# Kernel optimization log

Measured on AMD Instinct MI355X. Metric: run time of the kernel, lower is better.

The kernel has to match this reference:

```python
import jax, jax.numpy as jnp
import numpy as np

N_SRC = 50000   # source nodes in the block
N_DST = 50000   # destination nodes
E = 800000      # edges (avg in-degree 16, every dst has >=1 edge)
D = 256         # hidden_dim
V = 50000       # vocab_size
C = 104         # n_classes (POJ-104)


def setup_inputs() -> dict:
    key = jax.random.key(0)
    k1, k2, k3, k4, k5, k6 = jax.random.split(key, 6)
    token_id = jax.random.randint(k1, (N_SRC,), 0, V, dtype=jnp.int32)
    src_idx = jax.random.randint(k2, (E,), 0, N_SRC, dtype=jnp.int32)
    # every dst node gets at least one in-edge (DGL raises on 0-in-degree),
    # remaining edges land on random dst nodes; sorted so edges are grouped by dst
    extra = jax.random.randint(k3, (E - N_DST,), 0, N_DST, dtype=jnp.int32)
    dst_idx = jnp.sort(jnp.concatenate([jnp.arange(N_DST, dtype=jnp.int32), extra]))
    emb = jax.random.normal(k4, (V, D), dtype=jnp.float32)  # nn.Embedding default N(0,1)
    W = jax.random.normal(k5, (D, D), dtype=jnp.float32) / jnp.sqrt(D)
    b = jnp.zeros((D,), dtype=jnp.float32)
    Wc = jax.random.normal(k6, (C, D), dtype=jnp.float32) / jnp.sqrt(D)
    bc = jnp.zeros((C,), dtype=jnp.float32)
    return {"emb": emb, "W": W, "b": b, "Wc": Wc, "bc": bc,
            "token_id": token_id, "src_idx": src_idx, "dst_idx": dst_idx}


def reference(emb, W, b, Wc, bc, token_id, src_idx, dst_idx):
    # embedding gather for source nodes (first_layer branch)
    feat_src = emb[token_id]                  # [N_SRC, D]
    # message: copy_u -> mailbox messages per edge
    msgs = feat_src[src_idx]                  # [E, D]
    # per-dst segment stats (dst_idx is sorted / grouped by dst)
    deg = jax.ops.segment_sum(jnp.ones((E,), dtype=jnp.int32), dst_idx,
                              num_segments=N_DST)            # [N_DST]
    sum_all = jax.ops.segment_sum(msgs, dst_idx, num_segments=N_DST)  # [N_DST, D]
    # DGL mailbox reducer: last message in the segment is the 'current input',
    # the rest are children summed through CodeRNNCell: x = cur + relu(W @ sum_children + b)
    last_idx = jnp.cumsum(deg) - 1            # index of last edge per dst segment
    last_msg = msgs[last_idx]                 # [N_DST, D]
    child_sum = sum_all - last_msg            # sum of msgs excluding the last one
    rnn_out = last_msg + jax.nn.relu(child_sum @ W.T + b)
    # length == 1 segments bypass the RNN cell entirely: ft = the single message
    ft = jnp.where((deg == 1)[:, None], last_msg, rnn_out)   # [N_DST, D]
    # final classifier
    return ft @ Wc.T + bc                     # [N_DST, C]
```

## Files before the change

kernel.cpp:

```cpp
#include <hip/hip_runtime.h>
#include <hip/hip_bf16.h>

#define DD 256
#define CC 104

typedef __bf16 bf16x8 __attribute__((ext_vector_type(8)));
typedef float  f32x4  __attribute__((ext_vector_type(4)));

__device__ inline float bu2f(unsigned short u) {
    return __uint_as_float(((unsigned)u) << 16);
}
__device__ inline unsigned short f2bu(float f) {
    __hip_bfloat16 h = __float2bfloat16(f);
    return *reinterpret_cast<unsigned short*>(&h);
}

__global__ void prep_all(
    const int* __restrict__ token_id,
    const int* __restrict__ src_idx,
    const int* __restrict__ dst_idx,
    int* __restrict__ seg_start,
    int* __restrict__ seg_end,
    int* __restrict__ edge_tok,
    int E, int PB,
    const float* __restrict__ W,
    const float* __restrict__ Wc,
    __hip_bfloat16* __restrict__ Wfrag,
    __hip_bfloat16* __restrict__ Wcfrag)
{
    const int b = blockIdx.x;
    const int t = threadIdx.x;
    if (b < PB) {
        int e = b * 256 + t;
        if (e >= E) return;
        int d = dst_idx[e];
        edge_tok[e] = token_id[src_idx[e]];
        if (e == 0 || dst_idx[e - 1] != d) seg_start[d] = e;
        if (e == E - 1 || dst_idx[e + 1] != d) seg_end[d] = e + 1;
        return;
    }
    if (b < PB + 32) {
        int idx  = (b - PB) * 256 + t;
        int lane = idx & 63, g = idx >> 6;
        int nt = g & 15, k0 = g >> 4;
        int r = nt * 16 + (lane & 15);
        int c = k0 * 32 + (lane >> 4) * 8;
        const float* src = W + (size_t)r * DD + c;
        float4 v0 = *(const float4*)(src);
        float4 v1 = *(const float4*)(src + 4);
        uint4 pk;
        pk.x = (unsigned)f2bu(v0.x) | ((unsigned)f2bu(v0.y) << 16);
        pk.y = (unsigned)f2bu(v0.z) | ((unsigned)f2bu(v0.w) << 16);
        pk.z = (unsigned)f2bu(v1.x) | ((unsigned)f2bu(v1.y) << 16);
        pk.w = (unsigned)f2bu(v1.z) | ((unsigned)f2bu(v1.w) << 16);
        *(uint4*)(Wfrag + (size_t)idx * 8) = pk;
        return;
    }
    {
        int idx  = (b - PB - 32) * 256 + t;
        int lane = idx & 63, g = idx >> 6;
        int nt = g & 7, k0 = g >> 3;
        int r = nt * 16 + (lane & 15);
        int c = k0 * 32 + (lane >> 4) * 8;
        float4 v0 = make_float4(0.f,0.f,0.f,0.f);
        float4 v1 = make_float4(0.f,0.f,0.f,0.f);
        if (r < CC) {
            const float* src = Wc + (size_t)r * DD + c;
            v0 = *(const float4*)(src);
            v1 = *(const float4*)(src + 4);
        }
        uint4 pk;
        pk.x = (unsigned)f2bu(v0.x) | ((unsigned)f2bu(v0.y) << 16);
        pk.y = (unsigned)f2bu(v0.z) | ((unsigned)f2bu(v0.w) << 16);
        pk.z = (unsigned)f2bu(v1.x) | ((unsigned)f2bu(v1.y) << 16);
        pk.w = (unsigned)f2bu(v1.z) | ((unsigned)f2bu(v1.w) << 16);
        *(uint4*)(Wcfrag + (size_t)idx * 8) = pk;
    }
}

__global__ __launch_bounds__(256, 3) void we_gemm(
    const float* __restrict__ emb,
    const __hip_bfloat16* __restrict__ Wfrag,
    __hip_bfloat16* __restrict__ Webuf,
    __hip_bfloat16* __restrict__ embb,
    int V)
{
    __shared__ __hip_bfloat16 lds[32 * 512];
    const int t    = threadIdx.x;
    const int lane = t & 63;
    const int w    = t >> 6;
    const int quad = lane >> 4;
    const int l16  = lane & 15;
    const int mrow = blockIdx.x * 64 + w * 16 + l16;
    const int row  = min(mrow, V - 1);

    bf16x8 bfrag[8];
#pragma unroll
    for (int k0 = 0; k0 < 8; ++k0) {
        const float* src = emb + (size_t)row * DD + k0 * 32 + quad * 8;
        float4 v0 = *(const float4*)(src);
        float4 v1 = *(const float4*)(src + 4);
        uint4 pk;
        pk.x = (unsigned)f2bu(v0.x) | ((unsigned)f2bu(v0.y) << 16);
        pk.y = (unsigned)f2bu(v0.z) | ((unsigned)f2bu(v0.w) << 16);
        pk.z = (unsigned)f2bu(v1.x) | ((unsigned)f2bu(v1.y) << 16);
        pk.w = (unsigned)f2bu(v1.z) | ((unsigned)f2bu(v1.w) << 16);
        bfrag[k0] = *(bf16x8*)&pk;
        if (mrow < V)
            *(uint4*)(embb + (size_t)row * DD + k0 * 32 + quad * 8) = pk;
    }

    f32x4 acc[16];
#pragma unroll
    for (int nt = 0; nt < 16; ++nt) acc[nt] = (f32x4){0.f,0.f,0.f,0.f};

    for (int p = 0; p < 4; ++p) {
        if (p) __syncthreads();
#pragma unroll
        for (int it = 0; it < 8; ++it) {
            int idx = it * 256 + t;
            *(uint4*)(lds + (size_t)idx * 8) =
                *(const uint4*)(Wfrag + (size_t)p * 16384 + (size_t)idx * 8);
        }
        __syncthreads();
#pragma unroll
        for (int kl = 0; kl < 2; ++kl) {
            int k0 = p * 2 + kl;
#pragma unroll
            for (int nt = 0; nt < 16; ++nt) {
                bf16x8 wf = *(const bf16x8*)(lds + (kl * 16 + nt) * 512 + lane * 8);
                acc[nt] = __builtin_amdgcn_mfma_f32_16x16x32_bf16(wf, bfrag[k0], acc[nt], 0, 0, 0);
            }
        }
    }

    if (mrow < V) {
#pragma unroll
        for (int nt = 0; nt < 16; ++nt) {
            ushort4 o;
            o.x = f2bu(acc[nt][0]);
            o.y = f2bu(acc[nt][1]);
            o.z = f2bu(acc[nt][2]);
            o.w = f2bu(acc[nt][3]);
            *(ushort4*)(Webuf + (size_t)mrow * DD + nt * 16 + quad * 4) = o;
        }
    }
}

__global__ __launch_bounds__(256, 8) void seg_rnn_kernel(
                               const __hip_bfloat16* __restrict__ Webuf,
                               const __hip_bfloat16* __restrict__ embb,
                               const int* __restrict__ edge_tok,
                               const int* __restrict__ seg_start,
                               const int* __restrict__ seg_end,
                               const float* __restrict__ bvec,
                               __hip_bfloat16* __restrict__ ftb,
                               int n_dst)
{
    int w = (blockIdx.x * blockDim.x + threadIdx.x) >> 6;
    int lane = threadIdx.x & 63;
    if (w >= n_dst) return;
    int h   = lane >> 5;
    int l32 = lane & 31;
    int s  = seg_start[w];
    int e  = seg_end[w];
    int n  = e - 1 - s;
    int lt = edge_tok[e - 1];
    uint4 lm = *(const uint4*)(embb + (size_t)lt * DD + l32 * 8);
    bool gate = n > 0;
    int nfast = n < 64 ? n : 64;
    float acc[8] = {0.f,0.f,0.f,0.f,0.f,0.f,0.f,0.f};

#pragma unroll
    for (int bb = 0; bb < 4; ++bb) {
        int base = bb * 16;
        if (nfast > base) {
            uint4 uu[8];
#pragma unroll
            for (int k = 0; k < 8; ++k) {
                int r  = base + 2 * k + h;
                int rc = r < n - 1 ? r : n - 1;
                int tk = edge_tok[s + rc];
                uu[k] = *(const uint4*)(Webuf + (size_t)tk * DD + l32 * 8);
            }
#pragma unroll
            for (int k = 0; k < 8; ++k) {
                int r = base + 2 * k + h;
                if (r < nfast) {
                    const unsigned* ud = (const unsigned*)&uu[k];
#pragma unroll
                    for (int d = 0; d < 4; ++d) {
                        acc[2*d]   += __uint_as_float(ud[d] << 16);
                        acc[2*d+1] += __uint_as_float(ud[d] & 0xffff0000u);
                    }
                }
            }
        }
    }
    for (int i = s + 64 + h; i < e - 1; i += 2) {
        int t0 = edge_tok[i];
        uint4 u = *(const uint4*)(Webuf + (size_t)t0 * DD + l32 * 8);
        const unsigned* ud = (const unsigned*)&u;
#pragma unroll
        for (int d = 0; d < 4; ++d) {
            acc[2*d]   += __uint_as_float(ud[d] << 16);
            acc[2*d+1] += __uint_as_float(ud[d] & 0xffff0000u);
        }
    }

#pragma unroll
    for (int j = 0; j < 8; ++j) acc[j] += __shfl_xor(acc[j], 32, 64);

    if (h == 0) {
        float4 b0 = *(const float4*)(bvec + l32 * 8);
        float4 b1 = *(const float4*)(bvec + l32 * 8 + 4);
        float bl[8] = {b0.x, b0.y, b0.z, b0.w, b1.x, b1.y, b1.z, b1.w};
        const unsigned* lmd = (const unsigned*)&lm;
        uint4 o;
        unsigned* od = (unsigned*)&o;
#pragma unroll
        for (int d = 0; d < 4; ++d) {
            float lo = __uint_as_float(lmd[d] << 16);
            float hi = __uint_as_float(lmd[d] & 0xffff0000u);
            float v0 = lo + (gate ? fmaxf(acc[2*d]   + bl[2*d],   0.f) : 0.f);
            float v1 = hi + (gate ? fmaxf(acc[2*d+1] + bl[2*d+1], 0.f) : 0.f);
            od[d] = (unsigned)f2bu(v0) | ((unsigned)f2bu(v1) << 16);
        }
        *(uint4*)(ftb + (size_t)w * DD + l32 * 8) = o;
    }
}

__global__ __launch_bounds__(256, 4) void cls_mfma(
    const __hip_bfloat16* __restrict__ ftb,
    const __hip_bfloat16* __restrict__ Wcfrag,
    const float* __restrict__ bc,
    float* __restrict__ out,
    int M)
{
    __shared__ __hip_bfloat16 lds[32 * 512];
    const int t    = threadIdx.x;
    const int lane = t & 63;
    const int w    = t >> 6;
    const int quad = lane >> 4;
    const int l16  = lane & 15;
    const int mw   = blockIdx.x * 64 + w * 16;

    int mrow = min(mw + l16, M - 1);
    bf16x8 ffrag[8];
    const __hip_bfloat16* arow = ftb + (size_t)mrow * DD + quad * 8;
#pragma unroll
    for (int k0 = 0; k0 < 8; ++k0)
        ffrag[k0] = *(const bf16x8*)(arow + k0 * 32);

    f32x4 acc[8];
#pragma unroll
    for (int nt = 0; nt < 8; ++nt) acc[nt] = (f32x4){0.f,0.f,0.f,0.f};

    for (int p = 0; p < 2; ++p) {
        if (p) __syncthreads();
#pragma unroll
        for (int it = 0; it < 8; ++it) {
            int idx = it * 256 + t;
            *(uint4*)(lds + (size_t)idx * 8) =
                *(const uint4*)(Wcfrag + (size_t)p * 16384 + (size_t)idx * 8);
        }
        __syncthreads();
#pragma unroll
        for (int kl = 0; kl < 4; ++kl) {
            int k0 = p * 4 + kl;
#pragma unroll
            for (int nt = 0; nt < 8; ++nt) {
                bf16x8 wf = *(const bf16x8*)(lds + (kl * 8 + nt) * 512 + lane * 8);
                acc[nt] = __builtin_amdgcn_mfma_f32_16x16x32_bf16(wf, ffrag[k0], acc[nt], 0, 0, 0);
            }
        }
    }

    int m = mw + l16;
    if (m < M) {
#pragma unroll
        for (int nt = 0; nt < 8; ++nt) {
            int c0 = nt * 16 + quad * 4;
            if (c0 <= 100) {
                float4 bia = *(const float4*)(bc + c0);
                float4 o;
                o.x = acc[nt][0] + bia.x;
                o.y = acc[nt][1] + bia.y;
                o.z = acc[nt][2] + bia.z;
                o.w = acc[nt][3] + bia.w;
                *(float4*)(out + (size_t)m * CC + c0) = o;
            }
        }
    }
}

extern "C" void kernel_launch(void* const* d_in, const int* in_sizes, int n_in,
                              void* d_out, int out_size, void* d_ws, size_t ws_size,
                              hipStream_t stream)
{
    const float* emb      = (const float*)d_in[0];
    const float* W        = (const float*)d_in[1];
    const float* bvec     = (const float*)d_in[2];
    const float* Wc       = (const float*)d_in[3];
    const float* bc       = (const float*)d_in[4];
    const int*   token_id = (const int*)d_in[5];
    const int*   src_idx  = (const int*)d_in[6];
    const int*   dst_idx  = (const int*)d_in[7];
    float*       out      = (float*)d_out;

    const int E     = in_sizes[6];
    const int Vemb  = in_sizes[0] / DD;
    const int n_dst = out_size / CC;
    (void)n_in; (void)ws_size;

    char* ws = (char*)d_ws;
    size_t off = 0;
    auto alloc = [&](size_t bytes) {
        void* p = ws + off;
        off = (off + bytes + 255) & ~(size_t)255;
        return p;
    };
    int* seg_start = (int*)alloc((size_t)n_dst * sizeof(int));
    int* seg_end   = (int*)alloc((size_t)n_dst * sizeof(int));
    int* edge_tok  = (int*)alloc((size_t)E * sizeof(int));
    __hip_bfloat16* embb   = (__hip_bfloat16*)alloc((size_t)Vemb * DD * 2);
    __hip_bfloat16* Webuf  = (__hip_bfloat16*)alloc((size_t)Vemb * DD * 2);
    __hip_bfloat16* ftb    = (__hip_bfloat16*)alloc((size_t)n_dst * DD * 2);
    __hip_bfloat16* Wfrag  = (__hip_bfloat16*)alloc((size_t)128 * 512 * 2);
    __hip_bfloat16* Wcfrag = (__hip_bfloat16*)alloc((size_t)64 * 512 * 2);

    const int PB = (E + 255) / 256;
    const int we_blocks  = (Vemb + 63) / 64;
    const int cls_blocks = (n_dst + 63) / 64;

    prep_all<<<PB + 48, 256, 0, stream>>>(
        token_id, src_idx, dst_idx, seg_start, seg_end, edge_tok, E, PB,
        W, Wc, Wfrag, Wcfrag);
    we_gemm<<<we_blocks, 256, 0, stream>>>(
        emb, Wfrag, Webuf, embb, Vemb);
    seg_rnn_kernel<<<(n_dst + 3) / 4, 256, 0, stream>>>(
        Webuf, embb, edge_tok, seg_start, seg_end, bvec, ftb, n_dst);
    cls_mfma<<<cls_blocks, 256, 0, stream>>>(
        ftb, Wcfrag, bc, out, n_dst);
}
```

Measured before the change: 204.7 us.

## Slice feature tables into 32-column panels and gather per slice for L2 locality

Stores the transformed embedding table, bf16 embedding copy and the ft buffer in a column-sliced layout (eight panels of 32 columns each). The segment kernel now assigns each block one slice and has four lanes per destination node, so each panel's gather working set is smaller and may fit better in cache. The last token per segment is precomputed in prep, which saves a dependent load. The cost is that each edge token is reloaded eight times, one per slice, and there are more blocks with divergent loop lengths across the 16 nodes sharing a wave.

```diff
diff --git a/kernel.cpp b/kernel.cpp
--- a/kernel.cpp
+++ b/kernel.cpp
@@ -3,6 +3,7 @@
 
 #define DD 256
 #define CC 104
+#define NSL 8
 
 typedef __bf16 bf16x8 __attribute__((ext_vector_type(8)));
 typedef float  f32x4  __attribute__((ext_vector_type(4)));
@@ -22,6 +23,7 @@
     int* __restrict__ seg_start,
     int* __restrict__ seg_end,
     int* __restrict__ edge_tok,
+    int* __restrict__ last_tok,
     int E, int PB,
     const float* __restrict__ W,
     const float* __restrict__ Wc,
@@ -34,9 +36,10 @@
         int e = b * 256 + t;
         if (e >= E) return;
         int d = dst_idx[e];
-        edge_tok[e] = token_id[src_idx[e]];
+        int tok = token_id[src_idx[e]];
+        edge_tok[e] = tok;
         if (e == 0 || dst_idx[e - 1] != d) seg_start[d] = e;
-        if (e == E - 1 || dst_idx[e + 1] != d) seg_end[d] = e + 1;
+        if (e == E - 1 || dst_idx[e + 1] != d) { seg_end[d] = e + 1; last_tok[d] = tok; }
         return;
     }
     if (b < PB + 32) {
@@ -107,7 +110,7 @@
         pk.w = (unsigned)f2bu(v1.z) | ((unsigned)f2bu(v1.w) << 16);
         bfrag[k0] = *(bf16x8*)&pk;
         if (mrow < V)
-            *(uint4*)(embb + (size_t)row * DD + k0 * 32 + quad * 8) = pk;
+            *(uint4*)(embb + (size_t)k0 * V * 32 + (size_t)row * 32 + quad * 8) = pk;
     }
 
     f32x4 acc[16];
@@ -137,97 +140,93 @@
     if (mrow < V) {
 #pragma unroll
         for (int nt = 0; nt < 16; ++nt) {
+            int c0 = nt * 16 + quad * 4;
             ushort4 o;
             o.x = f2bu(acc[nt][0]);
             o.y = f2bu(acc[nt][1]);
             o.z = f2bu(acc[nt][2]);
             o.w = f2bu(acc[nt][3]);
-            *(ushort4*)(Webuf + (size_t)mrow * DD + nt * 16 + quad * 4) = o;
+            *(ushort4*)(Webuf + (size_t)(c0 >> 5) * V * 32 +
+                        (size_t)mrow * 32 + (c0 & 31)) = o;
         }
     }
 }
 
 __global__ __launch_bounds__(256, 8) void seg_rnn_kernel(
-                               const __hip_bfloat16* __restrict__ Webuf,
-                               const __hip_bfloat16* __restrict__ embb,
-                               const int* __restrict__ edge_tok,
-                               const int* __restrict__ seg_start,
-                               const int* __restrict__ seg_end,
-                               const float* __restrict__ bvec,
-                               __hip_bfloat16* __restrict__ ftb,
-                               int n_dst)
-{
-    int w = (blockIdx.x * blockDim.x + threadIdx.x) >> 6;
-    int lane = threadIdx.x & 63;
-    if (w >= n_dst) return;
-    int h   = lane >> 5;
-    int l32 = lane & 31;
-    int s  = seg_start[w];
-    int e  = seg_end[w];
-    int n  = e - 1 - s;
-    int lt = edge_tok[e - 1];
-    uint4 lm = *(const uint4*)(embb + (size_t)lt * DD + l32 * 8);
+    const __hip_bfloat16* __restrict__ Webuf,
+    const __hip_bfloat16* __restrict__ embb,
+    const int* __restrict__ edge_tok,
+    const int* __restrict__ seg_start,
+    const int* __restrict__ seg_end,
+    const int* __restrict__ last_tok,
+    const float* __restrict__ bvec,
+    __hip_bfloat16* __restrict__ ftb,
+    int n_dst, int V)
+{
+    const int bid  = blockIdx.x;
+    const int sl   = bid & 7;
+    const int g    = bid >> 3;
+    const int t    = threadIdx.x;
+    const int wv   = t >> 6;
+    const int lane = t & 63;
+    const int grp  = lane >> 2;
+    const int c    = lane & 3;
+
+    int d = g * 64 + wv * 16 + grp;
+    bool dok = d < n_dst;
+    int dc = dok ? d : n_dst - 1;
+    int s  = seg_start[dc];
+    int e  = seg_end[dc];
+    int lt = last_tok[dc];
+    int n  = dok ? (e - 1 - s) : 0;
+
+    const __hip_bfloat16* wsl = Webuf + (size_t)sl * V * 32;
+    const __hip_bfloat16* esl = embb  + (size_t)sl * V * 32;
+    uint4 lm = *(const uint4*)(esl + (size_t)lt * 32 + c * 8);
+
+    float acc[8] = {0.f,0.f,0.f,0.f,0.f,0.f,0.f,0.f};
+
+    for (int j = 0; ; j += 2) {
+        bool a0 = j < n, a1 = j + 1 < n;
+        if (!__any(a0)) break;
+        uint4 u0 = make_uint4(0u,0u,0u,0u);
+        uint4 u1 = make_uint4(0u,0u,0u,0u);
+        if (a0) {
+            int t0 = edge_tok[s + j];
+            u0 = *(const uint4*)(wsl + (size_t)t0 * 32 + c * 8);
+        }
+        if (a1) {
+            int t1 = edge_tok[s + j + 1];
+            u1 = *(const uint4*)(wsl + (size_t)t1 * 32 + c * 8);
+        }
+        const unsigned* p0 = (const unsigned*)&u0;
+        const unsigned* p1 = (const unsigned*)&u1;
+#pragma unroll
+        for (int k = 0; k < 4; ++k) {
+            acc[2*k]   += __uint_as_float(p0[k] << 16)
+                        + __uint_as_float(p1[k] << 16);
+            acc[2*k+1] += __uint_as_float(p0[k] & 0xffff0000u)
+                        + __uint_as_float(p1[k] & 0xffff0000u);
+        }
+    }
+
     bool gate = n > 0;
-    int nfast = n < 64 ? n : 64;
-    float acc[8] = {0.f,0.f,0.f,0.f,0.f,0.f,0.f,0.f};
-
-#pragma unroll
-    for (int bb = 0; bb < 4; ++bb) {
-        int base = bb * 16;
-        if (nfast > base) {
-            uint4 uu[8];
-#pragma unroll
-            for (int k = 0; k < 8; ++k) {
-                int r  = base + 2 * k + h;
-                int rc = r < n - 1 ? r : n - 1;
-                int tk = edge_tok[s + rc];
-                uu[k] = *(const uint4*)(Webuf + (size_t)tk * DD + l32 * 8);
-            }
-#pragma unroll
-            for (int k = 0; k < 8; ++k) {
-                int r = base + 2 * k + h;
-                if (r < nfast) {
-                    const unsigned* ud = (const unsigned*)&uu[k];
-#pragma unroll
-                    for (int d = 0; d < 4; ++d) {
-                        acc[2*d]   += __uint_as_float(ud[d] << 16);
-                        acc[2*d+1] += __uint_as_float(ud[d] & 0xffff0000u);
-                    }
-                }
-            }
-        }
-    }
-    for (int i = s + 64 + h; i < e - 1; i += 2) {
-        int t0 = edge_tok[i];
-        uint4 u = *(const uint4*)(Webuf + (size_t)t0 * DD + l32 * 8);
-        const unsigned* ud = (const unsigned*)&u;
-#pragma unroll
-        for (int d = 0; d < 4; ++d) {
-            acc[2*d]   += __uint_as_float(ud[d] << 16);
-            acc[2*d+1] += __uint_as_float(ud[d] & 0xffff0000u);
-        }
-    }
-
-#pragma unroll
-    for (int j = 0; j < 8; ++j) acc[j] += __shfl_xor(acc[j], 32, 64);
-
-    if (h == 0) {
-        float4 b0 = *(const float4*)(bvec + l32 * 8);
-        float4 b1 = *(const float4*)(bvec + l32 * 8 + 4);
-        float bl[8] = {b0.x, b0.y, b0.z, b0.w, b1.x, b1.y, b1.z, b1.w};
-        const unsigned* lmd = (const unsigned*)&lm;
-        uint4 o;
-        unsigned* od = (unsigned*)&o;
-#pragma unroll
-        for (int d = 0; d < 4; ++d) {
-            float lo = __uint_as_float(lmd[d] << 16);
-            float hi = __uint_as_float(lmd[d] & 0xffff0000u);
-            float v0 = lo + (gate ? fmaxf(acc[2*d]   + bl[2*d],   0.f) : 0.f);
-            float v1 = hi + (gate ? fmaxf(acc[2*d+1] + bl[2*d+1], 0.f) : 0.f);
-            od[d] = (unsigned)f2bu(v0) | ((unsigned)f2bu(v1) << 16);
-        }
-        *(uint4*)(ftb + (size_t)w * DD + l32 * 8) = o;
-    }
+    float4 b0 = *(const float4*)(bvec + sl * 32 + c * 8);
+    float4 b1 = *(const float4*)(bvec + sl * 32 + c * 8 + 4);
+    float bl[8] = {b0.x, b0.y, b0.z, b0.w, b1.x, b1.y, b1.z, b1.w};
+    const unsigned* lmd = (const unsigned*)&lm;
+    uint4 o;
+    unsigned* od = (unsigned*)&o;
+#pragma unroll
+    for (int k = 0; k < 4; ++k) {
+        float lo = __uint_as_float(lmd[k] << 16);
+        float hi = __uint_as_float(lmd[k] & 0xffff0000u);
+        float v0 = lo + (gate ? fmaxf(acc[2*k]   + bl[2*k],   0.f) : 0.f);
+        float v1 = hi + (gate ? fmaxf(acc[2*k+1] + bl[2*k+1], 0.f) : 0.f);
+        od[k] = (unsigned)f2bu(v0) | ((unsigned)f2bu(v1) << 16);
+    }
+    if (dok)
+        *(uint4*)(ftb + (size_t)sl * n_dst * 32 + (size_t)d * 32 + c * 8) = o;
 }
 
 __global__ __launch_bounds__(256, 4) void cls_mfma(
@@ -247,10 +246,10 @@
 
     int mrow = min(mw + l16, M - 1);
     bf16x8 ffrag[8];
-    const __hip_bfloat16* arow = ftb + (size_t)mrow * DD + quad * 8;
 #pragma unroll
     for (int k0 = 0; k0 < 8; ++k0)
-        ffrag[k0] = *(const bf16x8*)(arow + k0 * 32);
+        ffrag[k0] = *(const bf16x8*)(ftb + (size_t)k0 * M * 32 +
+                                     (size_t)mrow * 32 + quad * 8);
 
     f32x4 acc[8];
 #pragma unroll
@@ -322,6 +321,7 @@
     };
     int* seg_start = (int*)alloc((size_t)n_dst * sizeof(int));
     int* seg_end   = (int*)alloc((size_t)n_dst * sizeof(int));
+    int* last_tok  = (int*)alloc((size_t)n_dst * sizeof(int));
     int* edge_tok  = (int*)alloc((size_t)E * sizeof(int));
     __hip_bfloat16* embb   = (__hip_bfloat16*)alloc((size_t)Vemb * DD * 2);
     __hip_bfloat16* Webuf  = (__hip_bfloat16*)alloc((size_t)Vemb * DD * 2);
@@ -331,15 +331,17 @@
 
     const int PB = (E + 255) / 256;
     const int we_blocks  = (Vemb + 63) / 64;
+    const int seg_blocks = NSL * ((n_dst + 63) / 64);
     const int cls_blocks = (n_dst + 63) / 64;
 
     prep_all<<<PB + 48, 256, 0, stream>>>(
-        token_id, src_idx, dst_idx, seg_start, seg_end, edge_tok, E, PB,
+        token_id, src_idx, dst_idx, seg_start, seg_end, edge_tok, last_tok, E, PB,
         W, Wc, Wfrag, Wcfrag);
     we_gemm<<<we_blocks, 256, 0, stream>>>(
         emb, Wfrag, Webuf, embb, Vemb);
-    seg_rnn_kernel<<<(n_dst + 3) / 4, 256, 0, stream>>>(
-        Webuf, embb, edge_tok, seg_start, seg_end, bvec, ftb, n_dst);
+    seg_rnn_kernel<<<seg_blocks, 256, 0, stream>>>(
+        Webuf, embb, edge_tok, seg_start, seg_end, last_tok, bvec, ftb,
+        n_dst, Vemb);
     cls_mfma<<<cls_blocks, 256, 0, stream>>>(
         ftb, Wcfrag, bc, out, n_dst);
 }
```

Measured after the change: 199.9 us. 1.02x faster.
